# Performance work log

Measured on AMD Instinct MI355X. Metric: run time of the kernel, lower is better.

## Reference

```python
import jax, jax.numpy as jnp
import numpy as np

N_NODES, N_EDGES, F_IN = 8192, 32768, 16
N_SUB, N_GRAPH = 512, 32
EDGE_DIM, HID = 5, 128
DIMS = [(16, 32), (32, 64), (64, 64)]  # (M_in, M_out) per NNConv layer


def _segment_mean(x, seg, n):
    s = jax.ops.segment_sum(x, seg, num_segments=n)
    c = jax.ops.segment_sum(jnp.ones((x.shape[0], 1), x.dtype), seg, num_segments=n)
    return s / jnp.maximum(c, 1.0)


def _nnconv(x, src, dst, eattr, W1, b1, W2, b2, root, bias):
    # edge MLP -> per-edge weight matrix theta: [E, M_in, M_out]
    h = jax.nn.relu(eattr @ W1 + b1)
    theta = (h @ W2 + b2).reshape(-1, x.shape[1], root.shape[1])
    msg = jnp.einsum('ei,eio->eo', x[src], theta)          # gather + per-edge matvec
    agg = jax.ops.segment_sum(msg, dst, num_segments=x.shape[0])  # scatter-add (aggr='add')
    return agg + x @ root + bias


def setup_inputs() -> dict:
    key = jax.random.key(0)
    ks = jax.random.split(key, 32)
    inp = {}
    inp['x'] = jax.random.normal(ks[0], (N_NODES, F_IN), jnp.float32)
    inp['edge_index'] = jax.random.randint(ks[1], (2, N_EDGES), 0, N_NODES)
    inp['edge_attr'] = jax.random.uniform(ks[2], (N_EDGES, EDGE_DIM), jnp.float32)
    inp['node_to_subgraph'] = jnp.sort(jax.random.randint(ks[3], (N_NODES,), 0, N_SUB))
    inp['subgraph_to_graph'] = jnp.sort(jax.random.randint(ks[4], (N_SUB,), 0, N_GRAPH))
    i = 5
    for l, (ci, co) in enumerate(DIMS):
        inp[f'W1_{l}'] = jax.random.normal(ks[i], (EDGE_DIM, HID), jnp.float32) * 0.1
        inp[f'b1_{l}'] = jnp.zeros((HID,), jnp.float32)
        inp[f'W2_{l}'] = jax.random.normal(ks[i + 1], (HID, ci * co), jnp.float32) * 0.05
        inp[f'b2_{l}'] = jnp.zeros((ci * co,), jnp.float32)
        inp[f'root_{l}'] = jax.random.normal(ks[i + 2], (ci, co), jnp.float32) * 0.1
        inp[f'bias_{l}'] = jnp.zeros((co,), jnp.float32)
        i += 3
    inp['fc1_w'] = jax.random.normal(ks[i], (64, 32), jnp.float32) * 0.1
    inp['fc1_b'] = jnp.zeros((32,), jnp.float32)
    inp['fc2_w'] = jax.random.normal(ks[i + 1], (32, 16), jnp.float32) * 0.1
    inp['fc2_b'] = jnp.zeros((16,), jnp.float32)
    inp['fc3_w'] = jax.random.normal(ks[i + 2], (16, 1), jnp.float32) * 0.1
    inp['fc3_b'] = jnp.zeros((1,), jnp.float32)
    return inp


def reference(x, edge_index, edge_attr, node_to_subgraph, subgraph_to_graph,
              W1_0, b1_0, W2_0, b2_0, root_0, bias_0,
              W1_1, b1_1, W2_1, b2_1, root_1, bias_1,
              W1_2, b1_2, W2_2, b2_2, root_2, bias_2,
              fc1_w, fc1_b, fc2_w, fc2_b, fc3_w, fc3_b):
    src, dst = edge_index[0], edge_index[1]
    layers = [(W1_0, b1_0, W2_0, b2_0, root_0, bias_0),
              (W1_1, b1_1, W2_1, b2_1, root_1, bias_1),
              (W1_2, b1_2, W2_2, b2_2, root_2, bias_2)]
    h = x
    for (W1, b1, W2, b2, root, bias) in layers:
        h = jax.nn.elu(_nnconv(h, src, dst, edge_attr, W1, b1, W2, b2, root, bias))
    h = _segment_mean(h, node_to_subgraph, N_SUB)      # global_mean_pool over subgraphs
    h = _segment_mean(h, subgraph_to_graph, N_GRAPH)   # global_mean_pool over graphs
    h = jax.nn.elu(h @ fc1_w + fc1_b)
    h = jax.nn.elu(h @ fc2_w + fc2_b)
    return (h @ fc3_w + fc3_b).reshape(-1)
```

## Files before the change

kernel.cpp:

```cpp
#include <hip/hip_runtime.h>

#define E_EDGES 32768
#define NN 8192
#define HID 128
#define KS 4

typedef _Float16 half8 __attribute__((ext_vector_type(8)));
typedef _Float16 half4 __attribute__((ext_vector_type(4)));
typedef float f32x4 __attribute__((ext_vector_type(4)));

__global__ void zero_init_k(int* __restrict__ hist, float* __restrict__ pools, int npool) {
  int t = blockIdx.x * 256 + threadIdx.x;
  if (t < NN) hist[t] = 0;
  if (t < npool) pools[t] = 0.f;
}

__global__ void hist_k(const int* __restrict__ dst, int* __restrict__ hist) {
  int e = blockIdx.x * 256 + threadIdx.x;
  if (e < E_EDGES) atomicAdd(&hist[dst[e]], 1);
}

__global__ void scan_k(const int* __restrict__ hist, int* __restrict__ roff, int* __restrict__ cursor) {
  __shared__ int ps[1024];
  int t = threadIdx.x;
  int loc[8]; int s = 0;
  int base = t * 8;
#pragma unroll
  for (int j = 0; j < 8; ++j) { loc[j] = s; s += hist[base + j]; }
  ps[t] = s;
  __syncthreads();
  for (int off = 1; off < 1024; off <<= 1) {
    int v = 0;
    if (t >= off) v = ps[t - off];
    __syncthreads();
    if (t >= off) ps[t] += v;
    __syncthreads();
  }
  int excl = (t == 0) ? 0 : ps[t - 1];
#pragma unroll
  for (int j = 0; j < 8; ++j) { int v = excl + loc[j]; roff[base + j] = v; cursor[base + j] = v; }
  if (t == 1023) roff[NN] = ps[1023];
}

__global__ void scatter_k(const int* __restrict__ dst, int* __restrict__ cursor, int* __restrict__ eidx) {
  int e = blockIdx.x * 256 + threadIdx.x;
  if (e < E_EDGES) { int p = atomicAdd(&cursor[dst[e]], 1); eidx[p] = e; }
}

template <int CI, int CO>
__device__ inline void prep_b_one(int idx, const float* __restrict__ W2,
                                  const float* __restrict__ b2, _Float16* __restrict__ out) {
  constexpr int Kmain = 128 * CI;
  int j = idx & 7;
  int n = (idx >> 3) & (CO - 1);
  int kg = idx >> (3 + (CO == 64 ? 6 : 5));
  int k = kg * 8 + j;
  float v = 0.f;
  if (k < Kmain) {
    int h = k / CI, i = k & (CI - 1);
    v = W2[(h * CI + i) * CO + n];
  } else if (k < Kmain + CI) {
    int tt = k - Kmain;
    v = b2[tt * CO + n];
  }
  out[idx] = (_Float16)v;
}

__global__ void prep_b_all_k(const float* __restrict__ W2_0, const float* __restrict__ b2_0, _Float16* __restrict__ o0,
                             const float* __restrict__ W2_1, const float* __restrict__ b2_1, _Float16* __restrict__ o1,
                             const float* __restrict__ W2_2, const float* __restrict__ b2_2, _Float16* __restrict__ o2) {
  constexpr int N0 = 2176 * 32;
  constexpr int N1 = 4224 * 64;
  constexpr int N2 = 8320 * 64;
  int idx = blockIdx.x * 256 + threadIdx.x;
  if (idx < N0) prep_b_one<16, 32>(idx, W2_0, b2_0, o0);
  else if (idx < N0 + N1) prep_b_one<32, 64>(idx - N0, W2_1, b2_1, o1);
  else if (idx < N0 + N1 + N2) prep_b_one<64, 64>(idx - N0 - N1, W2_2, b2_2, o2);
}

template <int CI, int CO>
__launch_bounds__(256, 2)
__global__ void msg_mfma_k(const float* __restrict__ xcur, const int* __restrict__ src,
                           const float* __restrict__ eattr, const float* __restrict__ W1,
                           const float* __restrict__ b1, const _Float16* __restrict__ Bsw,
                           float* __restrict__ msgbuf) {
  constexpr int ME = 256;
  constexpr int L2CI = (CI == 64) ? 6 : ((CI == 32) ? 5 : 4);
  constexpr int XSTR = CI + 8;
  constexpr int HSTR = 40;
  constexpr int FC = CO / 16;
  constexpr int C4 = CI / 4;
  constexpr int L2C4 = L2CI - 2;
  constexpr int NMAIN = CI / 4;
  constexpr int XPN = (CI == 64) ? 2 : 1;

  __shared__ _Float16 he_s[ME * HSTR];
  __shared__ _Float16 xs_s[ME * XSTR];
  __shared__ float ea_s[ME * 5];
  __shared__ float W1s[5 * 32];
  __shared__ float b1s[32];
  __shared__ int src_s[ME];

  int t = threadIdx.x;
  int e0 = blockIdx.x * ME;
  int y = blockIdx.y;
  int hbeg = y * 32;

  for (int j = t; j < ME * 5; j += 256) ea_s[j] = eattr[e0 * 5 + j];
  if (t < 5 * 32) W1s[t] = W1[(t >> 5) * HID + hbeg + (t & 31)];
  if (t < 32) b1s[t] = b1[hbeg + t];
  src_s[t] = src[e0 + t];
  __syncthreads();

  for (int j = t; j < 32 * ME; j += 256) {
    int hl = j >> 8, e = j & 255;
    float v = b1s[hl];
#pragma unroll
    for (int d = 0; d < 5; ++d) v += ea_s[e * 5 + d] * W1s[d * 32 + hl];
    he_s[e * HSTR + hl] = (_Float16)fmaxf(v, 0.f);
  }
  for (int j = t; j < ME * C4; j += 256) {
    int e = j >> L2C4, i4 = j & (C4 - 1);
    float4 v = ((const float4*)xcur)[src_s[e] * C4 + i4];
    half4 hq = {(_Float16)v.x, (_Float16)v.y, (_Float16)v.z, (_Float16)v.w};
    *(half4*)&xs_s[e * XSTR + i4 * 4] = hq;
  }
  __syncthreads();

  int lane = t & 63;
  int w = t >> 6;
  int quad = lane >> 4, l15 = lane & 15;
  int qsh = (quad >> 1) << 4;

  int cbeg = y * CI;
  int cend = cbeg + CI + ((y == 3) ? 4 : 0);

  const half8* bsw8 = (const half8*)Bsw;
  int ib = quad * CO + l15;

  half8 xp[4][XPN];
  const _Float16* hbp[4];
#pragma unroll
  for (int fr = 0; fr < 4; ++fr) {
    int e = w * 64 + fr * 16 + l15;
    int i0 = (CI == 16) ? ((quad & 1) * 8) : (quad * 8);
    xp[fr][0] = *(const half8*)&xs_s[e * XSTR + i0];
    if constexpr (CI == 64) xp[fr][1] = *(const half8*)&xs_s[e * XSTR + i0 + 32];
    hbp[fr] = he_s + e * HSTR;
  }

  f32x4 acc[4][FC];
#pragma unroll
  for (int fr = 0; fr < 4; ++fr)
#pragma unroll
    for (int fc = 0; fc < FC; ++fc)
#pragma unroll
      for (int r = 0; r < 4; ++r) acc[fr][fc][r] = 0.f;

  half8 breg[4][FC];
#pragma unroll
  for (int j = 0; j < 4; ++j)
#pragma unroll
    for (int fc = 0; fc < FC; ++fc)
      breg[j][fc] = bsw8[(cbeg + j) * 4 * CO + ib + fc * 16];

  for (int r = 0; r < NMAIN; ++r) {
    int c0 = cbeg + r * 4;
    unsigned int hp2[4];
    half4 hp4[4];
    if constexpr (CI == 64) {
      int oh = (c0 >> 1) - hbeg;
#pragma unroll
      for (int fr = 0; fr < 4; ++fr) hp2[fr] = *(const unsigned int*)(hbp[fr] + oh);
    } else if constexpr (CI == 32) {
      int oh = c0 - hbeg;
#pragma unroll
      for (int fr = 0; fr < 4; ++fr) hp4[fr] = *(const half4*)(hbp[fr] + oh);
    }
#pragma unroll
    for (int j = 0; j < 4; ++j) {
      int c = c0 + j;
      half8 a[4];
#pragma unroll
      for (int fr = 0; fr < 4; ++fr) {
        if constexpr (CI == 64) {
          unsigned short hb = (unsigned short)((j >= 2) ? (hp2[fr] >> 16) : hp2[fr]);
          _Float16 hv = __builtin_bit_cast(_Float16, hb);
          a[fr] = xp[fr][j & 1] * hv;
        } else if constexpr (CI == 32) {
          a[fr] = xp[fr][0] * hp4[fr][j];
        } else {
          unsigned int hw = *(const unsigned int*)(hbp[fr] + (2 * c - hbeg));
          _Float16 hv = __builtin_bit_cast(_Float16, (unsigned short)(hw >> qsh));
          a[fr] = xp[fr][0] * hv;
        }
      }
#pragma unroll
      for (int fc = 0; fc < FC; ++fc) {
#pragma unroll
        for (int fr = 0; fr < 4; ++fr)
          acc[fr][fc] = __builtin_amdgcn_mfma_f32_16x16x32_f16(a[fr], breg[j][fc], acc[fr][fc], 0, 0, 0);
      }
      int cn = c + 4;
      if (cn >= cend) cn = cend - 1;
#pragma unroll
      for (int fc = 0; fc < FC; ++fc)
        breg[j][fc] = bsw8[cn * 4 * CO + ib + fc * 16];
    }
  }

  if (y == 3) {
#pragma unroll
    for (int j = 0; j < 4; ++j) {
      half8 a[4];
#pragma unroll
      for (int fr = 0; fr < 4; ++fr) a[fr] = xp[fr][(CI == 64) ? (j & 1) : 0];
#pragma unroll
      for (int fc = 0; fc < FC; ++fc) {
#pragma unroll
        for (int fr = 0; fr < 4; ++fr)
          acc[fr][fc] = __builtin_amdgcn_mfma_f32_16x16x32_f16(a[fr], breg[j][fc], acc[fr][fc], 0, 0, 0);
      }
    }
  }

  float* mb = msgbuf + ((size_t)y * E_EDGES + e0) * CO;
#pragma unroll
  for (int fr = 0; fr < 4; ++fr)
#pragma unroll
    for (int fc = 0; fc < FC; ++fc)
#pragma unroll
      for (int r = 0; r < 4; ++r) {
        int el = w * 64 + fr * 16 + quad * 4 + r;
        int o = fc * 16 + l15;
        mb[el * CO + o] = acc[fr][fc][r];
      }
}

template <int CI, int CO, bool POOL>
__global__ void gather_elu_k(const float* __restrict__ xcur, const float* __restrict__ root,
                             const float* __restrict__ bias, const float* __restrict__ msgbuf,
                             const int* __restrict__ roff, const int* __restrict__ eidx,
                             float* __restrict__ xnext, const int* __restrict__ n2s,
                             float* __restrict__ ssum, float* __restrict__ scnt) {
  constexpr int NB = 256 / CO;
  __shared__ float xs[NB * CI];
  int t = threadIdx.x;
  int n0 = blockIdx.x * NB;
  for (int j = t; j < NB * CI; j += 256) xs[j] = xcur[n0 * CI + j];
  __syncthreads();
  int nl = t / CO, o = t & (CO - 1);
  int n = n0 + nl;
  float a = bias[o];
#pragma unroll
  for (int i = 0; i < CI; ++i) a += xs[nl * CI + i] * root[i * CO + o];
  int j1 = roff[n + 1];
  for (int j = roff[n]; j < j1; ++j) {
    int e = eidx[j];
    float m = 0.f;
#pragma unroll
    for (int s = 0; s < KS; ++s) m += msgbuf[((size_t)s * E_EDGES + e) * CO + o];
    a += m;
  }
  float v = a > 0.f ? a : expm1f(a);
  if constexpr (POOL) {
    int s = n2s[n];
    atomicAdd(&ssum[(s << 6) + o], v);
    if (o == 0) atomicAdd(&scnt[s], 1.f);
  } else {
    xnext[n * CO + o] = v;
  }
}

__global__ void pg_head_k(const float* __restrict__ ssum, const float* __restrict__ scnt,
                          const int* __restrict__ s2g,
                          const float* __restrict__ w1, const float* __restrict__ b1,
                          const float* __restrict__ w2, const float* __restrict__ b2,
                          const float* __restrict__ w3, const float* __restrict__ b3,
                          float* __restrict__ out) {
  int g = blockIdx.x;
  int t = threadIdx.x;
  __shared__ int s2s[512];
  __shared__ float hm[64], h1[32], h2[16];
  for (int i = t; i < 512; i += 64) s2s[i] = s2g[i];
  __syncthreads();
  float acc = 0.f, cnt = 0.f;
  for (int s = 0; s < 512; ++s) {
    if (s2s[s] == g) {
      acc += ssum[(s << 6) + t] / fmaxf(scnt[s], 1.f);
      cnt += 1.f;
    }
  }
  hm[t] = acc / fmaxf(cnt, 1.f);
  __syncthreads();
  if (t < 32) {
    float a = b1[t];
    for (int i = 0; i < 64; ++i) a += hm[i] * w1[i * 32 + t];
    h1[t] = a > 0.f ? a : expm1f(a);
  }
  __syncthreads();
  if (t < 16) {
    float a = b2[t];
    for (int i = 0; i < 32; ++i) a += h1[i] * w2[i * 16 + t];
    h2[t] = a > 0.f ? a : expm1f(a);
  }
  __syncthreads();
  if (t == 0) {
    float a = b3[0];
    for (int i = 0; i < 16; ++i) a += h2[i] * w3[i];
    out[g] = a;
  }
}

extern "C" void kernel_launch(void* const* d_in, const int* in_sizes, int n_in,
                              void* d_out, int out_size, void* d_ws, size_t ws_size,
                              hipStream_t stream) {
  (void)in_sizes; (void)n_in; (void)out_size; (void)ws_size;
  const float* x0 = (const float*)d_in[0];
  const int* ei = (const int*)d_in[1];
  const float* ea = (const float*)d_in[2];
  const int* n2s = (const int*)d_in[3];
  const int* s2g = (const int*)d_in[4];
  const float* W1_[3] = {(const float*)d_in[5], (const float*)d_in[11], (const float*)d_in[17]};
  const float* b1_[3] = {(const float*)d_in[6], (const float*)d_in[12], (const float*)d_in[18]};
  const float* W2_[3] = {(const float*)d_in[7], (const float*)d_in[13], (const float*)d_in[19]};
  const float* b2_[3] = {(const float*)d_in[8], (const float*)d_in[14], (const float*)d_in[20]};
  const float* rt_[3] = {(const float*)d_in[9], (const float*)d_in[15], (const float*)d_in[21]};
  const float* bs_[3] = {(const float*)d_in[10], (const float*)d_in[16], (const float*)d_in[22]};
  const float* fc1w = (const float*)d_in[23]; const float* fc1b = (const float*)d_in[24];
  const float* fc2w = (const float*)d_in[25]; const float* fc2b = (const float*)d_in[26];
  const float* fc3w = (const float*)d_in[27]; const float* fc3b = (const float*)d_in[28];
  float* out = (float*)d_out;

  const int* srcp = ei;
  const int* dstp = ei + E_EDGES;

  char* wsb = (char*)d_ws;
  size_t off = 0;
  auto alloc = [&](size_t bytes) {
    void* p = wsb + off;
    off += (bytes + 255) & ~(size_t)255;
    return p;
  };
  _Float16* Bsw0 = (_Float16*)alloc((size_t)2176 * 32 * 2);
  _Float16* Bsw1 = (_Float16*)alloc((size_t)4224 * 64 * 2);
  _Float16* Bsw2 = (_Float16*)alloc((size_t)8320 * 64 * 2);
  float* msgbuf = (float*)alloc((size_t)KS * E_EDGES * 64 * 4);
  float* x1 = (float*)alloc((size_t)NN * 32 * 4);
  float* x2 = (float*)alloc((size_t)NN * 64 * 4);
  int* hist = (int*)alloc((size_t)NN * 4);
  int* roff = (int*)alloc((size_t)(NN + 1) * 4);
  int* cursor = (int*)alloc((size_t)NN * 4);
  int* eidx = (int*)alloc((size_t)E_EDGES * 4);
  const int npool = 512 * 64 + 512;
  float* pools = (float*)alloc((size_t)npool * 4);
  float* ssum = pools;
  float* scnt = pools + 512 * 64;

  zero_init_k<<<(npool + 255) / 256, 256, 0, stream>>>(hist, pools, npool);
  hist_k<<<E_EDGES / 256, 256, 0, stream>>>(dstp, hist);
  scan_k<<<1, 1024, 0, stream>>>(hist, roff, cursor);
  scatter_k<<<E_EDGES / 256, 256, 0, stream>>>(dstp, cursor, eidx);
  prep_b_all_k<<<(2176 * 32 + 4224 * 64 + 8320 * 64) / 256, 256, 0, stream>>>(
      W2_[0], b2_[0], Bsw0, W2_[1], b2_[1], Bsw1, W2_[2], b2_[2], Bsw2);

  dim3 mg(E_EDGES / 256, KS);
  msg_mfma_k<16, 32><<<mg, 256, 0, stream>>>(x0, srcp, ea, W1_[0], b1_[0], Bsw0, msgbuf);
  gather_elu_k<16, 32, false><<<NN / 8, 256, 0, stream>>>(x0, rt_[0], bs_[0], msgbuf, roff, eidx, x1, nullptr, nullptr, nullptr);
  msg_mfma_k<32, 64><<<mg, 256, 0, stream>>>(x1, srcp, ea, W1_[1], b1_[1], Bsw1, msgbuf);
  gather_elu_k<32, 64, false><<<NN / 4, 256, 0, stream>>>(x1, rt_[1], bs_[1], msgbuf, roff, eidx, x2, nullptr, nullptr, nullptr);
  msg_mfma_k<64, 64><<<mg, 256, 0, stream>>>(x2, srcp, ea, W1_[2], b1_[2], Bsw2, msgbuf);
  gather_elu_k<64, 64, true><<<NN / 4, 256, 0, stream>>>(x2, rt_[2], bs_[2], msgbuf, roff, eidx, nullptr, n2s, ssum, scnt);

  pg_head_k<<<32, 64, 0, stream>>>(ssum, scnt, s2g, fc1w, fc1b, fc2w, fc2b, fc3w, fc3b, out);
}
```

Before: 286.5 us.

## Replace CSR build and message buffer with atomic scatter-add into node aggregates

The edge kernel now atomically adds its per-edge messages directly into a per-node aggregate buffer indexed by destination, instead of writing a KS-split message buffer that a separate gather kernel reduced through a CSR built with histogram, scan and scatter kernels. This removes three preprocessing launches and the large message-buffer write and reread, and the node kernel just reads the aggregate. In exchange it issues many float atomics to global memory (one per output element per K-split), which can contend and makes the summation order nondeterministic. The hidden-activation loop index mapping was also swapped to reduce LDS bank conflicts.

```diff
diff --git a/kernel.cpp b/kernel.cpp
--- a/kernel.cpp
+++ b/kernel.cpp
@@ -9,42 +9,9 @@
 typedef _Float16 half4 __attribute__((ext_vector_type(4)));
 typedef float f32x4 __attribute__((ext_vector_type(4)));
 
-__global__ void zero_init_k(int* __restrict__ hist, float* __restrict__ pools, int npool) {
-  int t = blockIdx.x * 256 + threadIdx.x;
-  if (t < NN) hist[t] = 0;
-  if (t < npool) pools[t] = 0.f;
-}
-
-__global__ void hist_k(const int* __restrict__ dst, int* __restrict__ hist) {
-  int e = blockIdx.x * 256 + threadIdx.x;
-  if (e < E_EDGES) atomicAdd(&hist[dst[e]], 1);
-}
-
-__global__ void scan_k(const int* __restrict__ hist, int* __restrict__ roff, int* __restrict__ cursor) {
-  __shared__ int ps[1024];
-  int t = threadIdx.x;
-  int loc[8]; int s = 0;
-  int base = t * 8;
-#pragma unroll
-  for (int j = 0; j < 8; ++j) { loc[j] = s; s += hist[base + j]; }
-  ps[t] = s;
-  __syncthreads();
-  for (int off = 1; off < 1024; off <<= 1) {
-    int v = 0;
-    if (t >= off) v = ps[t - off];
-    __syncthreads();
-    if (t >= off) ps[t] += v;
-    __syncthreads();
-  }
-  int excl = (t == 0) ? 0 : ps[t - 1];
-#pragma unroll
-  for (int j = 0; j < 8; ++j) { int v = excl + loc[j]; roff[base + j] = v; cursor[base + j] = v; }
-  if (t == 1023) roff[NN] = ps[1023];
-}
-
-__global__ void scatter_k(const int* __restrict__ dst, int* __restrict__ cursor, int* __restrict__ eidx) {
-  int e = blockIdx.x * 256 + threadIdx.x;
-  if (e < E_EDGES) { int p = atomicAdd(&cursor[dst[e]], 1); eidx[p] = e; }
+__global__ void zero_all_k(float4* __restrict__ p, int n4) {
+  int i = blockIdx.x * 256 + threadIdx.x;
+  if (i < n4) p[i] = float4{0.f, 0.f, 0.f, 0.f};
 }
 
 template <int CI, int CO>
@@ -81,9 +48,10 @@
 template <int CI, int CO>
 __launch_bounds__(256, 2)
 __global__ void msg_mfma_k(const float* __restrict__ xcur, const int* __restrict__ src,
+                           const int* __restrict__ dst,
                            const float* __restrict__ eattr, const float* __restrict__ W1,
                            const float* __restrict__ b1, const _Float16* __restrict__ Bsw,
-                           float* __restrict__ msgbuf) {
+                           float* __restrict__ agg) {
   constexpr int ME = 256;
   constexpr int L2CI = (CI == 64) ? 6 : ((CI == 32) ? 5 : 4);
   constexpr int XSTR = CI + 8;
@@ -100,6 +68,7 @@
   __shared__ float W1s[5 * 32];
   __shared__ float b1s[32];
   __shared__ int src_s[ME];
+  __shared__ int dst_s[ME];
 
   int t = threadIdx.x;
   int e0 = blockIdx.x * ME;
@@ -110,10 +79,11 @@
   if (t < 5 * 32) W1s[t] = W1[(t >> 5) * HID + hbeg + (t & 31)];
   if (t < 32) b1s[t] = b1[hbeg + t];
   src_s[t] = src[e0 + t];
+  dst_s[t] = dst[e0 + t];
   __syncthreads();
 
   for (int j = t; j < 32 * ME; j += 256) {
-    int hl = j >> 8, e = j & 255;
+    int hl = j & 31, e = j >> 5;
     float v = b1s[hl];
 #pragma unroll
     for (int d = 0; d < 5; ++d) v += ea_s[e * 5 + d] * W1s[d * 32 + hl];
@@ -224,25 +194,26 @@
     }
   }
 
-  float* mb = msgbuf + ((size_t)y * E_EDGES + e0) * CO;
-#pragma unroll
-  for (int fr = 0; fr < 4; ++fr)
+#pragma unroll
+  for (int fr = 0; fr < 4; ++fr) {
+    int dcache[4];
+#pragma unroll
+    for (int r = 0; r < 4; ++r) dcache[r] = dst_s[w * 64 + fr * 16 + quad * 4 + r];
 #pragma unroll
     for (int fc = 0; fc < FC; ++fc)
 #pragma unroll
       for (int r = 0; r < 4; ++r) {
-        int el = w * 64 + fr * 16 + quad * 4 + r;
         int o = fc * 16 + l15;
-        mb[el * CO + o] = acc[fr][fc][r];
+        atomicAdd(&agg[(size_t)dcache[r] * CO + o], acc[fr][fc][r]);
       }
+  }
 }
 
 template <int CI, int CO, bool POOL>
-__global__ void gather_elu_k(const float* __restrict__ xcur, const float* __restrict__ root,
-                             const float* __restrict__ bias, const float* __restrict__ msgbuf,
-                             const int* __restrict__ roff, const int* __restrict__ eidx,
-                             float* __restrict__ xnext, const int* __restrict__ n2s,
-                             float* __restrict__ ssum, float* __restrict__ scnt) {
+__global__ void node_elu_k(const float* __restrict__ xcur, const float* __restrict__ root,
+                           const float* __restrict__ bias, const float* __restrict__ agg,
+                           float* __restrict__ xnext, const int* __restrict__ n2s,
+                           float* __restrict__ ssum, float* __restrict__ scnt) {
   constexpr int NB = 256 / CO;
   __shared__ float xs[NB * CI];
   int t = threadIdx.x;
@@ -251,17 +222,9 @@
   __syncthreads();
   int nl = t / CO, o = t & (CO - 1);
   int n = n0 + nl;
-  float a = bias[o];
+  float a = bias[o] + agg[(size_t)n * CO + o];
 #pragma unroll
   for (int i = 0; i < CI; ++i) a += xs[nl * CI + i] * root[i * CO + o];
-  int j1 = roff[n + 1];
-  for (int j = roff[n]; j < j1; ++j) {
-    int e = eidx[j];
-    float m = 0.f;
-#pragma unroll
-    for (int s = 0; s < KS; ++s) m += msgbuf[((size_t)s * E_EDGES + e) * CO + o];
-    a += m;
-  }
   float v = a > 0.f ? a : expm1f(a);
   if constexpr (POOL) {
     int s = n2s[n];
@@ -345,32 +308,30 @@
   _Float16* Bsw0 = (_Float16*)alloc((size_t)2176 * 32 * 2);
   _Float16* Bsw1 = (_Float16*)alloc((size_t)4224 * 64 * 2);
   _Float16* Bsw2 = (_Float16*)alloc((size_t)8320 * 64 * 2);
-  float* msgbuf = (float*)alloc((size_t)KS * E_EDGES * 64 * 4);
+  const int npool = 512 * 64 + 512;
+  const int nagg0 = NN * 32, nagg1 = NN * 64, nagg2 = NN * 64;
+  const int nzero = npool + nagg0 + nagg1 + nagg2;
+  float* zbase = (float*)alloc((size_t)nzero * 4);
+  float* ssum = zbase;
+  float* scnt = zbase + 512 * 64;
+  float* agg0 = zbase + npool;
+  float* agg1 = agg0 + nagg0;
+  float* agg2 = agg1 + nagg1;
   float* x1 = (float*)alloc((size_t)NN * 32 * 4);
   float* x2 = (float*)alloc((size_t)NN * 64 * 4);
-  int* hist = (int*)alloc((size_t)NN * 4);
-  int* roff = (int*)alloc((size_t)(NN + 1) * 4);
-  int* cursor = (int*)alloc((size_t)NN * 4);
-  int* eidx = (int*)alloc((size_t)E_EDGES * 4);
-  const int npool = 512 * 64 + 512;
-  float* pools = (float*)alloc((size_t)npool * 4);
-  float* ssum = pools;
-  float* scnt = pools + 512 * 64;
-
-  zero_init_k<<<(npool + 255) / 256, 256, 0, stream>>>(hist, pools, npool);
-  hist_k<<<E_EDGES / 256, 256, 0, stream>>>(dstp, hist);
-  scan_k<<<1, 1024, 0, stream>>>(hist, roff, cursor);
-  scatter_k<<<E_EDGES / 256, 256, 0, stream>>>(dstp, cursor, eidx);
+
+  const int n4 = nzero / 4;
+  zero_all_k<<<(n4 + 255) / 256, 256, 0, stream>>>((float4*)zbase, n4);
   prep_b_all_k<<<(2176 * 32 + 4224 * 64 + 8320 * 64) / 256, 256, 0, stream>>>(
       W2_[0], b2_[0], Bsw0, W2_[1], b2_[1], Bsw1, W2_[2], b2_[2], Bsw2);
 
   dim3 mg(E_EDGES / 256, KS);
-  msg_mfma_k<16, 32><<<mg, 256, 0, stream>>>(x0, srcp, ea, W1_[0], b1_[0], Bsw0, msgbuf);
-  gather_elu_k<16, 32, false><<<NN / 8, 256, 0, stream>>>(x0, rt_[0], bs_[0], msgbuf, roff, eidx, x1, nullptr, nullptr, nullptr);
-  msg_mfma_k<32, 64><<<mg, 256, 0, stream>>>(x1, srcp, ea, W1_[1], b1_[1], Bsw1, msgbuf);
-  gather_elu_k<32, 64, false><<<NN / 4, 256, 0, stream>>>(x1, rt_[1], bs_[1], msgbuf, roff, eidx, x2, nullptr, nullptr, nullptr);
-  msg_mfma_k<64, 64><<<mg, 256, 0, stream>>>(x2, srcp, ea, W1_[2], b1_[2], Bsw2, msgbuf);
-  gather_elu_k<64, 64, true><<<NN / 4, 256, 0, stream>>>(x2, rt_[2], bs_[2], msgbuf, roff, eidx, nullptr, n2s, ssum, scnt);
+  msg_mfma_k<16, 32><<<mg, 256, 0, stream>>>(x0, srcp, dstp, ea, W1_[0], b1_[0], Bsw0, agg0);
+  node_elu_k<16, 32, false><<<NN / 8, 256, 0, stream>>>(x0, rt_[0], bs_[0], agg0, x1, nullptr, nullptr, nullptr);
+  msg_mfma_k<32, 64><<<mg, 256, 0, stream>>>(x1, srcp, dstp, ea, W1_[1], b1_[1], Bsw1, agg1);
+  node_elu_k<32, 64, false><<<NN / 4, 256, 0, stream>>>(x1, rt_[1], bs_[1], agg1, x2, nullptr, nullptr, nullptr);
+  msg_mfma_k<64, 64><<<mg, 256, 0, stream>>>(x2, srcp, dstp, ea, W1_[2], b1_[2], Bsw2, agg2);
+  node_elu_k<64, 64, true><<<NN / 4, 256, 0, stream>>>(x2, rt_[2], bs_[2], agg2, nullptr, n2s, ssum, scnt);
 
   pg_head_k<<<32, 64, 0, stream>>>(ssum, scnt, s2g, fc1w, fc1b, fc2w, fc2b, fc3w, fc3b, out);
 }
```

Result: slower. 299.5 us (+4.5%).

## Halve edges per block, gather x directly into registers, shrink B prefetch

Applied to the files above, without the earlier changes.

The message kernel now handles 128 edges per block instead of 256, with 2 fragments per wave instead of 4. It drops the shared-memory staging of gathered source features and loads them from global memory straight into registers. The B-operand prefetch depth shrinks from 4 to 2 slots and launch bounds rise to 4 blocks per SM. Together these aim to cut register and LDS use so more waves are resident to hide latency. The cost is less reuse of each B fragment per load and twice as many blocks re-reading Bsw.

```diff
diff --git a/kernel.cpp b/kernel.cpp
--- a/kernel.cpp
+++ b/kernel.cpp
@@ -78,24 +78,26 @@
   else if (idx < N0 + N1 + N2) prep_b_one<64, 64>(idx - N0 - N1, W2_2, b2_2, o2);
 }
 
+__device__ inline half8 pack8(float4 a, float4 b) {
+  half8 r;
+  r[0] = (_Float16)a.x; r[1] = (_Float16)a.y; r[2] = (_Float16)a.z; r[3] = (_Float16)a.w;
+  r[4] = (_Float16)b.x; r[5] = (_Float16)b.y; r[6] = (_Float16)b.z; r[7] = (_Float16)b.w;
+  return r;
+}
+
 template <int CI, int CO>
-__launch_bounds__(256, 2)
+__launch_bounds__(256, 4)
 __global__ void msg_mfma_k(const float* __restrict__ xcur, const int* __restrict__ src,
                            const float* __restrict__ eattr, const float* __restrict__ W1,
                            const float* __restrict__ b1, const _Float16* __restrict__ Bsw,
                            float* __restrict__ msgbuf) {
-  constexpr int ME = 256;
-  constexpr int L2CI = (CI == 64) ? 6 : ((CI == 32) ? 5 : 4);
-  constexpr int XSTR = CI + 8;
-  constexpr int HSTR = 40;
+  constexpr int ME = 128;
+  constexpr int HSTR = 36;
   constexpr int FC = CO / 16;
-  constexpr int C4 = CI / 4;
-  constexpr int L2C4 = L2CI - 2;
   constexpr int NMAIN = CI / 4;
   constexpr int XPN = (CI == 64) ? 2 : 1;
 
   __shared__ _Float16 he_s[ME * HSTR];
-  __shared__ _Float16 xs_s[ME * XSTR];
   __shared__ float ea_s[ME * 5];
   __shared__ float W1s[5 * 32];
   __shared__ float b1s[32];
@@ -109,21 +111,15 @@
   for (int j = t; j < ME * 5; j += 256) ea_s[j] = eattr[e0 * 5 + j];
   if (t < 5 * 32) W1s[t] = W1[(t >> 5) * HID + hbeg + (t & 31)];
   if (t < 32) b1s[t] = b1[hbeg + t];
-  src_s[t] = src[e0 + t];
+  if (t < ME) src_s[t] = src[e0 + t];
   __syncthreads();
 
   for (int j = t; j < 32 * ME; j += 256) {
-    int hl = j >> 8, e = j & 255;
+    int hl = j & 31, e = j >> 5;
     float v = b1s[hl];
 #pragma unroll
     for (int d = 0; d < 5; ++d) v += ea_s[e * 5 + d] * W1s[d * 32 + hl];
     he_s[e * HSTR + hl] = (_Float16)fmaxf(v, 0.f);
-  }
-  for (int j = t; j < ME * C4; j += 256) {
-    int e = j >> L2C4, i4 = j & (C4 - 1);
-    float4 v = ((const float4*)xcur)[src_s[e] * C4 + i4];
-    half4 hq = {(_Float16)v.x, (_Float16)v.y, (_Float16)v.z, (_Float16)v.w};
-    *(half4*)&xs_s[e * XSTR + i4 * 4] = hq;
   }
   __syncthreads();
 
@@ -138,51 +134,59 @@
   const half8* bsw8 = (const half8*)Bsw;
   int ib = quad * CO + l15;
 
-  half8 xp[4][XPN];
-  const _Float16* hbp[4];
-#pragma unroll
-  for (int fr = 0; fr < 4; ++fr) {
-    int e = w * 64 + fr * 16 + l15;
+  half8 xp[2][XPN];
+  const _Float16* hbp[2];
+#pragma unroll
+  for (int fr = 0; fr < 2; ++fr) {
+    int e = w * 32 + fr * 16 + l15;
+    const float* xr = xcur + (size_t)src_s[e] * CI;
     int i0 = (CI == 16) ? ((quad & 1) * 8) : (quad * 8);
-    xp[fr][0] = *(const half8*)&xs_s[e * XSTR + i0];
-    if constexpr (CI == 64) xp[fr][1] = *(const half8*)&xs_s[e * XSTR + i0 + 32];
+    float4 v0 = *(const float4*)(xr + i0);
+    float4 v1 = *(const float4*)(xr + i0 + 4);
+    xp[fr][0] = pack8(v0, v1);
+    if constexpr (CI == 64) {
+      float4 v2 = *(const float4*)(xr + i0 + 32);
+      float4 v3 = *(const float4*)(xr + i0 + 36);
+      xp[fr][1] = pack8(v2, v3);
+    }
     hbp[fr] = he_s + e * HSTR;
   }
 
-  f32x4 acc[4][FC];
-#pragma unroll
-  for (int fr = 0; fr < 4; ++fr)
+  f32x4 acc[2][FC];
+#pragma unroll
+  for (int fr = 0; fr < 2; ++fr)
 #pragma unroll
     for (int fc = 0; fc < FC; ++fc)
 #pragma unroll
       for (int r = 0; r < 4; ++r) acc[fr][fc][r] = 0.f;
 
-  half8 breg[4][FC];
-#pragma unroll
-  for (int j = 0; j < 4; ++j)
+  half8 breg[2][FC];
+#pragma unroll
+  for (int sl = 0; sl < 2; ++sl)
 #pragma unroll
     for (int fc = 0; fc < FC; ++fc)
-      breg[j][fc] = bsw8[(cbeg + j) * 4 * CO + ib + fc * 16];
+      breg[sl][fc] = bsw8[(cbeg + sl) * 4 * CO + ib + fc * 16];
 
   for (int r = 0; r < NMAIN; ++r) {
     int c0 = cbeg + r * 4;
-    unsigned int hp2[4];
-    half4 hp4[4];
+    unsigned int hp2[2];
+    half4 hp4[2];
     if constexpr (CI == 64) {
       int oh = (c0 >> 1) - hbeg;
 #pragma unroll
-      for (int fr = 0; fr < 4; ++fr) hp2[fr] = *(const unsigned int*)(hbp[fr] + oh);
+      for (int fr = 0; fr < 2; ++fr) hp2[fr] = *(const unsigned int*)(hbp[fr] + oh);
     } else if constexpr (CI == 32) {
       int oh = c0 - hbeg;
 #pragma unroll
-      for (int fr = 0; fr < 4; ++fr) hp4[fr] = *(const half4*)(hbp[fr] + oh);
+      for (int fr = 0; fr < 2; ++fr) hp4[fr] = *(const half4*)(hbp[fr] + oh);
     }
 #pragma unroll
     for (int j = 0; j < 4; ++j) {
       int c = c0 + j;
-      half8 a[4];
-#pragma unroll
-      for (int fr = 0; fr < 4; ++fr) {
+      int sl = j & 1;
+      half8 a[2];
+#pragma unroll
+      for (int fr = 0; fr < 2; ++fr) {
         if constexpr (CI == 64) {
           unsigned short hb = (unsigned short)((j >= 2) ? (hp2[fr] >> 16) : hp2[fr]);
           _Float16 hv = __builtin_bit_cast(_Float16, hb);
@@ -198,40 +202,46 @@
 #pragma unroll
       for (int fc = 0; fc < FC; ++fc) {
 #pragma unroll
-        for (int fr = 0; fr < 4; ++fr)
-          acc[fr][fc] = __builtin_amdgcn_mfma_f32_16x16x32_f16(a[fr], breg[j][fc], acc[fr][fc], 0, 0, 0);
+        for (int fr = 0; fr < 2; ++fr)
+          acc[fr][fc] = __builtin_amdgcn_mfma_f32_16x16x32_f16(a[fr], breg[sl][fc], acc[fr][fc], 0, 0, 0);
       }
-      int cn = c + 4;
+      int cn = c + 2;
       if (cn >= cend) cn = cend - 1;
 #pragma unroll
       for (int fc = 0; fc < FC; ++fc)
-        breg[j][fc] = bsw8[cn * 4 * CO + ib + fc * 16];
+        breg[sl][fc] = bsw8[cn * 4 * CO + ib + fc * 16];
     }
   }
 
   if (y == 3) {
 #pragma unroll
     for (int j = 0; j < 4; ++j) {
-      half8 a[4];
-#pragma unroll
-      for (int fr = 0; fr < 4; ++fr) a[fr] = xp[fr][(CI == 64) ? (j & 1) : 0];
+      int sl = j & 1;
+      half8 a[2];
+#pragma unroll
+      for (int fr = 0; fr < 2; ++fr) a[fr] = xp[fr][(CI == 64) ? (j & 1) : 0];
 #pragma unroll
       for (int fc = 0; fc < FC; ++fc) {
 #pragma unroll
-        for (int fr = 0; fr < 4; ++fr)
-          acc[fr][fc] = __builtin_amdgcn_mfma_f32_16x16x32_f16(a[fr], breg[j][fc], acc[fr][fc], 0, 0, 0);
+        for (int fr = 0; fr < 2; ++fr)
+          acc[fr][fc] = __builtin_amdgcn_mfma_f32_16x16x32_f16(a[fr], breg[sl][fc], acc[fr][fc], 0, 0, 0);
       }
+      int cn = cbeg + CI + j + 2;
+      if (cn >= cend) cn = cend - 1;
+#pragma unroll
+      for (int fc = 0; fc < FC; ++fc)
+        breg[sl][fc] = bsw8[cn * 4 * CO + ib + fc * 16];
     }
   }
 
   float* mb = msgbuf + ((size_t)y * E_EDGES + e0) * CO;
 #pragma unroll
-  for (int fr = 0; fr < 4; ++fr)
+  for (int fr = 0; fr < 2; ++fr)
 #pragma unroll
     for (int fc = 0; fc < FC; ++fc)
 #pragma unroll
       for (int r = 0; r < 4; ++r) {
-        int el = w * 64 + fr * 16 + quad * 4 + r;
+        int el = w * 32 + fr * 16 + quad * 4 + r;
         int o = fc * 16 + l15;
         mb[el * CO + o] = acc[fr][fc][r];
       }
@@ -364,7 +374,7 @@
   prep_b_all_k<<<(2176 * 32 + 4224 * 64 + 8320 * 64) / 256, 256, 0, stream>>>(
       W2_[0], b2_[0], Bsw0, W2_[1], b2_[1], Bsw1, W2_[2], b2_[2], Bsw2);
 
-  dim3 mg(E_EDGES / 256, KS);
+  dim3 mg(E_EDGES / 128, KS);
   msg_mfma_k<16, 32><<<mg, 256, 0, stream>>>(x0, srcp, ea, W1_[0], b1_[0], Bsw0, msgbuf);
   gather_elu_k<16, 32, false><<<NN / 8, 256, 0, stream>>>(x0, rt_[0], bs_[0], msgbuf, roff, eidx, x1, nullptr, nullptr, nullptr);
   msg_mfma_k<32, 64><<<mg, 256, 0, stream>>>(x1, srcp, ea, W1_[1], b1_[1], Bsw1, msgbuf);
```

Result: slower. 298.3 us (+4.1%).

## Double-buffer B weight tiles in LDS via async global_load_lds pipeline

Applied to the files above, without the earlier changes.

Reorders the prepared B matrix into lane-contiguous fragments and streams each 4-chunk group into a double-buffered LDS region with direct global-to-LDS loads, synchronized via vmcnt waits and barriers. This replaces the per-wave register prefetch of B from global memory, letting the four waves share one copy per block. Source-node features are now gathered straight into registers instead of being staged through LDS. The he_s stride shrinks and its fill loop is reindexed. The change adds two barriers per iteration and more LDS use, which may reduce occupancy.

```diff
diff --git a/kernel.cpp b/kernel.cpp
--- a/kernel.cpp
+++ b/kernel.cpp
@@ -51,18 +51,19 @@
 __device__ inline void prep_b_one(int idx, const float* __restrict__ W2,
                                   const float* __restrict__ b2, _Float16* __restrict__ out) {
   constexpr int Kmain = 128 * CI;
+  constexpr int FC = CO / 16;
   int j = idx & 7;
-  int n = (idx >> 3) & (CO - 1);
-  int kg = idx >> (3 + (CO == 64 ? 6 : 5));
-  int k = kg * 8 + j;
+  int h8 = idx >> 3;
+  int lane = h8 & 63;
+  int quad = lane >> 4, l15 = lane & 15;
+  int rest = h8 >> 6;
+  int fc = rest & (FC - 1);
+  int c = rest / FC;
+  int k = c * 32 + quad * 8 + j;
+  int n = fc * 16 + l15;
   float v = 0.f;
-  if (k < Kmain) {
-    int h = k / CI, i = k & (CI - 1);
-    v = W2[(h * CI + i) * CO + n];
-  } else if (k < Kmain + CI) {
-    int tt = k - Kmain;
-    v = b2[tt * CO + n];
-  }
+  if (k < Kmain) v = W2[(size_t)k * CO + n];
+  else if (k < Kmain + CI) v = b2[(k - Kmain) * CO + n];
   out[idx] = (_Float16)v;
 }
 
@@ -78,6 +79,19 @@
   else if (idx < N0 + N1 + N2) prep_b_one<64, 64>(idx - N0 - N1, W2_2, b2_2, o2);
 }
 
+__device__ inline half8 pack8(float4 a, float4 b) {
+  half8 r;
+  r[0] = (_Float16)a.x; r[1] = (_Float16)a.y; r[2] = (_Float16)a.z; r[3] = (_Float16)a.w;
+  r[4] = (_Float16)b.x; r[5] = (_Float16)b.y; r[6] = (_Float16)b.z; r[7] = (_Float16)b.w;
+  return r;
+}
+
+__device__ __forceinline__ void gload_lds16(const _Float16* g, _Float16* l) {
+  __builtin_amdgcn_global_load_lds(
+      (__attribute__((address_space(1))) void*)(size_t)(const void*)g,
+      (__attribute__((address_space(3))) void*)(size_t)(void*)l, 16, 0, 0);
+}
+
 template <int CI, int CO>
 __launch_bounds__(256, 2)
 __global__ void msg_mfma_k(const float* __restrict__ xcur, const int* __restrict__ src,
@@ -85,21 +99,18 @@
                            const float* __restrict__ b1, const _Float16* __restrict__ Bsw,
                            float* __restrict__ msgbuf) {
   constexpr int ME = 256;
-  constexpr int L2CI = (CI == 64) ? 6 : ((CI == 32) ? 5 : 4);
-  constexpr int XSTR = CI + 8;
-  constexpr int HSTR = 40;
+  constexpr int HSTR = 36;
   constexpr int FC = CO / 16;
-  constexpr int C4 = CI / 4;
-  constexpr int L2C4 = L2CI - 2;
   constexpr int NMAIN = CI / 4;
   constexpr int XPN = (CI == 64) ? 2 : 1;
+  constexpr int RHALF = 4 * FC * 64 * 8;
 
   __shared__ _Float16 he_s[ME * HSTR];
-  __shared__ _Float16 xs_s[ME * XSTR];
   __shared__ float ea_s[ME * 5];
   __shared__ float W1s[5 * 32];
   __shared__ float b1s[32];
   __shared__ int src_s[ME];
+  __shared__ _Float16 bls[2 * RHALF];
 
   int t = threadIdx.x;
   int e0 = blockIdx.x * ME;
@@ -113,17 +124,11 @@
   __syncthreads();
 
   for (int j = t; j < 32 * ME; j += 256) {
-    int hl = j >> 8, e = j & 255;
+    int hl = j & 31, e = j >> 5;
     float v = b1s[hl];
 #pragma unroll
     for (int d = 0; d < 5; ++d) v += ea_s[e * 5 + d] * W1s[d * 32 + hl];
     he_s[e * HSTR + hl] = (_Float16)fmaxf(v, 0.f);
-  }
-  for (int j = t; j < ME * C4; j += 256) {
-    int e = j >> L2C4, i4 = j & (C4 - 1);
-    float4 v = ((const float4*)xcur)[src_s[e] * C4 + i4];
-    half4 hq = {(_Float16)v.x, (_Float16)v.y, (_Float16)v.z, (_Float16)v.w};
-    *(half4*)&xs_s[e * XSTR + i4 * 4] = hq;
   }
   __syncthreads();
 
@@ -131,21 +136,24 @@
   int w = t >> 6;
   int quad = lane >> 4, l15 = lane & 15;
   int qsh = (quad >> 1) << 4;
-
-  int cbeg = y * CI;
-  int cend = cbeg + CI + ((y == 3) ? 4 : 0);
-
-  const half8* bsw8 = (const half8*)Bsw;
-  int ib = quad * CO + l15;
+  int Rg0 = y * NMAIN;
+  int NR = NMAIN + ((y == 3) ? 1 : 0);
 
   half8 xp[4][XPN];
   const _Float16* hbp[4];
 #pragma unroll
   for (int fr = 0; fr < 4; ++fr) {
     int e = w * 64 + fr * 16 + l15;
+    const float* xr = xcur + (size_t)src_s[e] * CI;
     int i0 = (CI == 16) ? ((quad & 1) * 8) : (quad * 8);
-    xp[fr][0] = *(const half8*)&xs_s[e * XSTR + i0];
-    if constexpr (CI == 64) xp[fr][1] = *(const half8*)&xs_s[e * XSTR + i0 + 32];
+    float4 v0 = *(const float4*)(xr + i0);
+    float4 v1 = *(const float4*)(xr + i0 + 4);
+    xp[fr][0] = pack8(v0, v1);
+    if constexpr (CI == 64) {
+      float4 v2 = *(const float4*)(xr + i0 + 32);
+      float4 v3 = *(const float4*)(xr + i0 + 36);
+      xp[fr][1] = pack8(v2, v3);
+    }
     hbp[fr] = he_s + e * HSTR;
   }
 
@@ -157,71 +165,86 @@
 #pragma unroll
       for (int r = 0; r < 4; ++r) acc[fr][fc][r] = 0.f;
 
-  half8 breg[4][FC];
-#pragma unroll
-  for (int j = 0; j < 4; ++j)
-#pragma unroll
-    for (int fc = 0; fc < FC; ++fc)
-      breg[j][fc] = bsw8[(cbeg + j) * 4 * CO + ib + fc * 16];
-
-  for (int r = 0; r < NMAIN; ++r) {
-    int c0 = cbeg + r * 4;
-    unsigned int hp2[4];
-    half4 hp4[4];
-    if constexpr (CI == 64) {
-      int oh = (c0 >> 1) - hbeg;
-#pragma unroll
-      for (int fr = 0; fr < 4; ++fr) hp2[fr] = *(const unsigned int*)(hbp[fr] + oh);
-    } else if constexpr (CI == 32) {
-      int oh = c0 - hbeg;
-#pragma unroll
-      for (int fr = 0; fr < 4; ++fr) hp4[fr] = *(const half4*)(hbp[fr] + oh);
+  auto stageR = [&](int rg, int buf) {
+    const _Float16* gb = Bsw + (size_t)rg * RHALF + w * (FC * 512);
+    _Float16* lb = bls + buf * RHALF + w * (FC * 512);
+#pragma unroll
+    for (int i = 0; i < FC; ++i)
+      gload_lds16(gb + i * 512 + lane * 8, lb + i * 512);
+  };
+
+  stageR(Rg0, 0);
+  stageR(Rg0 + 1, 1);
+
+  for (int r = 0; r < NR; ++r) {
+    if (r + 1 < NR) {
+      if constexpr (FC == 4) asm volatile("s_waitcnt vmcnt(4)" ::: "memory");
+      else                   asm volatile("s_waitcnt vmcnt(2)" ::: "memory");
+    } else {
+      asm volatile("s_waitcnt vmcnt(0)" ::: "memory");
     }
-#pragma unroll
-    for (int j = 0; j < 4; ++j) {
-      int c = c0 + j;
-      half8 a[4];
-#pragma unroll
-      for (int fr = 0; fr < 4; ++fr) {
-        if constexpr (CI == 64) {
-          unsigned short hb = (unsigned short)((j >= 2) ? (hp2[fr] >> 16) : hp2[fr]);
-          _Float16 hv = __builtin_bit_cast(_Float16, hb);
-          a[fr] = xp[fr][j & 1] * hv;
-        } else if constexpr (CI == 32) {
-          a[fr] = xp[fr][0] * hp4[fr][j];
-        } else {
-          unsigned int hw = *(const unsigned int*)(hbp[fr] + (2 * c - hbeg));
-          _Float16 hv = __builtin_bit_cast(_Float16, (unsigned short)(hw >> qsh));
-          a[fr] = xp[fr][0] * hv;
+    __builtin_amdgcn_s_barrier();
+
+    const _Float16* bp = bls + (r & 1) * RHALF;
+    int c0 = (Rg0 + r) * 4;
+
+    if (r < NMAIN) {
+      unsigned int hp2[4];
+      half4 hp4[4];
+      if constexpr (CI == 64) {
+        int oh = (c0 >> 1) - hbeg;
+#pragma unroll
+        for (int fr = 0; fr < 4; ++fr) hp2[fr] = *(const unsigned int*)(hbp[fr] + oh);
+      } else if constexpr (CI == 32) {
+        int oh = c0 - hbeg;
+#pragma unroll
+        for (int fr = 0; fr < 4; ++fr) hp4[fr] = *(const half4*)(hbp[fr] + oh);
+      }
+#pragma unroll
+      for (int cr = 0; cr < 4; ++cr) {
+        int c = c0 + cr;
+        half8 a[4];
+#pragma unroll
+        for (int fr = 0; fr < 4; ++fr) {
+          if constexpr (CI == 64) {
+            unsigned short hb = (unsigned short)((cr >= 2) ? (hp2[fr] >> 16) : hp2[fr]);
+            _Float16 hv = __builtin_bit_cast(_Float16, hb);
+            a[fr] = xp[fr][cr & 1] * hv;
+          } else if constexpr (CI == 32) {
+            a[fr] = xp[fr][0] * hp4[fr][cr];
+          } else {
+            unsigned int hw = *(const unsigned int*)(hbp[fr] + (2 * c - hbeg));
+            _Float16 hv = __builtin_bit_cast(_Float16, (unsigned short)(hw >> qsh));
+            a[fr] = xp[fr][0] * hv;
+          }
+        }
+#pragma unroll
+        for (int fc = 0; fc < FC; ++fc) {
+          half8 bf = *(const half8*)&bp[((cr * FC + fc) * 64 + lane) * 8];
+#pragma unroll
+          for (int fr = 0; fr < 4; ++fr)
+            acc[fr][fc] = __builtin_amdgcn_mfma_f32_16x16x32_f16(a[fr], bf, acc[fr][fc], 0, 0, 0);
         }
       }
-#pragma unroll
-      for (int fc = 0; fc < FC; ++fc) {
-#pragma unroll
-        for (int fr = 0; fr < 4; ++fr)
-          acc[fr][fc] = __builtin_amdgcn_mfma_f32_16x16x32_f16(a[fr], breg[j][fc], acc[fr][fc], 0, 0, 0);
-      }
-      int cn = c + 4;
-      if (cn >= cend) cn = cend - 1;
-#pragma unroll
-      for (int fc = 0; fc < FC; ++fc)
-        breg[j][fc] = bsw8[cn * 4 * CO + ib + fc * 16];
-    }
-  }
-
-  if (y == 3) {
-#pragma unroll
-    for (int j = 0; j < 4; ++j) {
-      half8 a[4];
-#pragma unroll
-      for (int fr = 0; fr < 4; ++fr) a[fr] = xp[fr][(CI == 64) ? (j & 1) : 0];
-#pragma unroll
-      for (int fc = 0; fc < FC; ++fc) {
-#pragma unroll
-        for (int fr = 0; fr < 4; ++fr)
-          acc[fr][fc] = __builtin_amdgcn_mfma_f32_16x16x32_f16(a[fr], breg[j][fc], acc[fr][fc], 0, 0, 0);
+    } else {
+#pragma unroll
+      for (int cr = 0; cr < 4; ++cr) {
+        half8 a[4];
+#pragma unroll
+        for (int fr = 0; fr < 4; ++fr) a[fr] = xp[fr][(CI == 64) ? (cr & 1) : 0];
+#pragma unroll
+        for (int fc = 0; fc < FC; ++fc) {
+          half8 bf = *(const half8*)&bp[((cr * FC + fc) * 64 + lane) * 8];
+#pragma unroll
+          for (int fr = 0; fr < 4; ++fr)
+            acc[fr][fc] = __builtin_amdgcn_mfma_f32_16x16x32_f16(a[fr], bf, acc[fr][fc], 0, 0, 0);
+        }
       }
     }
+
+    asm volatile("s_waitcnt lgkmcnt(0)" ::: "memory");
+    __builtin_amdgcn_s_barrier();
+    if (r + 2 < NR) stageR(Rg0 + r + 2, r & 1);
   }
 
   float* mb = msgbuf + ((size_t)y * E_EDGES + e0) * CO;
```

Result: faster. 278.3 us (-2.9%).
